# Kernel optimization log

Hardware: AMD Instinct MI355X
Metric: run time of the kernel (lower is better)

Reference implementation:

```python
import jax, jax.numpy as jnp
import numpy as np

N_NODES = 100000
N_EDGES = 1600000
IN_C, HID_C, OUT_C = 128, 128, 64


def setup_inputs() -> dict:
    key = jax.random.key(0)
    ks = jax.random.split(key, 8)
    x = jax.random.normal(ks[0], (N_NODES, IN_C), dtype=jnp.float32)
    edge_index = jax.random.randint(ks[1], (2, N_EDGES), 0, N_NODES, dtype=jnp.int32)
    # Glorot-ish init for GCNConv linear weights, zero bias (PyG default)
    def glorot(k, fan_in, fan_out):
        s = jnp.sqrt(6.0 / (fan_in + fan_out))
        return jax.random.uniform(k, (fan_in, fan_out), dtype=jnp.float32, minval=-s, maxval=s)
    return {
        "x": x,
        "edge_index": edge_index,
        "W1": glorot(ks[2], IN_C, HID_C), "b1": jnp.zeros((HID_C,), jnp.float32),
        "W2": glorot(ks[3], HID_C, HID_C), "b2": jnp.zeros((HID_C,), jnp.float32),
        "W3": glorot(ks[4], HID_C, OUT_C), "b3": jnp.zeros((OUT_C,), jnp.float32),
    }


def _gcn_norm(edge_index, num_nodes):
    # Add self-loops (PyG GCNConv default) and compute symmetric normalization
    loops = jnp.arange(num_nodes, dtype=edge_index.dtype)
    src = jnp.concatenate([edge_index[0], loops])  # [E+N]
    dst = jnp.concatenate([edge_index[1], loops])
    deg = jax.ops.segment_sum(jnp.ones_like(dst, dtype=jnp.float32), dst,
                              num_segments=num_nodes)
    deg_inv_sqrt = jnp.where(deg > 0, jax.lax.rsqrt(jnp.maximum(deg, 1.0)), 0.0)
    norm = deg_inv_sqrt[src] * deg_inv_sqrt[dst]  # [E+N]
    return src, dst, norm


def _gcn_layer(x, src, dst, norm, W, b, num_nodes):
    h = x @ W                                # [N, out] dense transform first
    msg = h[src] * norm[:, None]             # gather + scale  [E+N, out]
    out = jax.ops.segment_sum(msg, dst, num_segments=num_nodes)  # scatter-add
    return out + b


def reference(x, edge_index, W1, b1, W2, b2, W3, b3):
    n = x.shape[0]
    src, dst, norm = _gcn_norm(edge_index, n)
    h = jax.nn.relu(_gcn_layer(x, src, dst, norm, W1, b1, n))
    h = jax.nn.relu(_gcn_layer(h, src, dst, norm, W2, b2, n))
    return _gcn_layer(h, src, dst, norm, W3, b3, n)
```

## Files before the change

### kernel.cpp

```cpp
#include <hip/hip_runtime.h>

#define NN 100000
#define NE 1600000
#define NBK 98
#define BSH 10
#define MPAD 100096
#define SCB 391
#define CAP 20480

typedef unsigned short ushortT;
typedef unsigned long long ull;
using sh8 = __attribute__((ext_vector_type(8))) short;
using f4  = __attribute__((ext_vector_type(4))) float;


__device__ __forceinline__ unsigned short bfr(float f) {
  unsigned u = __float_as_uint(f);
  u += 0x7FFF + ((u >> 16) & 1);
  return (unsigned short)(u >> 16);
}
__device__ __forceinline__ float bf2f(unsigned short h) {
  return __uint_as_float(((unsigned)h) << 16);
}
__device__ __forceinline__ void acc8(const uint4 v, float* a) {
  a[0] += __uint_as_float(v.x << 16);
  a[1] += __uint_as_float(v.x & 0xFFFF0000u);
  a[2] += __uint_as_float(v.y << 16);
  a[3] += __uint_as_float(v.y & 0xFFFF0000u);
  a[4] += __uint_as_float(v.z << 16);
  a[5] += __uint_as_float(v.z & 0xFFFF0000u);
  a[6] += __uint_as_float(v.w << 16);
  a[7] += __uint_as_float(v.w & 0xFFFF0000u);
}
__device__ __forceinline__ sh8 hi8(const float4 a, const float4 b) {
  sh8 r;
  r[0] = (short)bfr(a.x); r[1] = (short)bfr(a.y);
  r[2] = (short)bfr(a.z); r[3] = (short)bfr(a.w);
  r[4] = (short)bfr(b.x); r[5] = (short)bfr(b.y);
  r[6] = (short)bfr(b.z); r[7] = (short)bfr(b.w);
  return r;
}


template <int COUT>
__device__ __forceinline__ void packone(const float* __restrict__ W,
                                        ushortT* __restrict__ Bp, int i) {
  const int j = i & 7;
  const int l = (i >> 3) & 63;
  const int rest = i >> 9;
  const int g = rest % (COUT / 16);
  const int ks = rest / (COUT / 16);
  const int k = (ks & 3) * 32 + (l >> 4) * 8 + j;
  const int n = g * 16 + (l & 15);
  const float v = W[k * COUT + n];
  const unsigned short h = bfr(v);
  Bp[i] = (ks < 4) ? h : bfr(v - bf2f(h));
}


__global__ __launch_bounds__(256) void k_scatterpack(
    const int* __restrict__ src, const int* __restrict__ dst,
    int* __restrict__ cursor, ull* __restrict__ pairArr,
    const float* __restrict__ W1, const float* __restrict__ W2,
    const float* __restrict__ W3, ushortT* __restrict__ Bp1,
    ushortT* __restrict__ Bp2, ushortT* __restrict__ Bp3) {
  if (blockIdx.x >= SCB) {
    const int i = (blockIdx.x - SCB) * 256 + threadIdx.x;
    if (i < 32768) packone<128>(W1, Bp1, i);
    else if (i < 65536) packone<128>(W2, Bp2, i - 32768);
    else packone<64>(W3, Bp3, i - 65536);
    return;
  }
  __shared__ int lcnt[NBK];
  __shared__ int lbase[NBK];
  __shared__ int lrank[NBK];
  __shared__ int bbase[NBK];
  __shared__ ull sorted[4096];
  __shared__ int target[4096];
  const int t = threadIdx.x;
  for (int i = t; i < NBK; i += 256) { lcnt[i] = 0; lrank[i] = 0; }
  __syncthreads();
  const int base = blockIdx.x * 4096;
  int rs[16], rd[16];
#pragma unroll
  for (int q = 0; q < 16; q++) {
    int e = base + t + 256 * q;
    rs[q] = (e < NE) ? src[e] : -1;
    rd[q] = (e < NE) ? dst[e] : -1;
    if (rd[q] >= 0) atomicAdd(&lcnt[rd[q] >> BSH], 1);
  }
  __syncthreads();
  if (t == 0) {
    int run = 0;
    for (int i = 0; i < NBK; i++) { lbase[i] = run; run += lcnt[i]; }
  }
  __syncthreads();
  if (t < NBK && lcnt[t] > 0) bbase[t] = atomicAdd(&cursor[t], lcnt[t]);
  __syncthreads();
#pragma unroll
  for (int q = 0; q < 16; q++) {
    if (rd[q] >= 0) {
      int b = rd[q] >> BSH;
      int r = atomicAdd(&lrank[b], 1);
      int slot = lbase[b] + r;
      sorted[slot] = ((ull)(unsigned)rs[q] << 32) | (unsigned)rd[q];
      target[slot] = b * CAP + bbase[b] + r;
    }
  }
  __syncthreads();
  const int n = min(4096, NE - base);
  for (int s = t; s < n; s += 256) pairArr[target[s]] = sorted[s];
}


__global__ __launch_bounds__(1024) void k_buildcsr(const ull* __restrict__ pairArr,
                                                   const int* __restrict__ cnt,
                                                   float* __restrict__ dinv,
                                                   int* __restrict__ rowptr,
                                                   int* __restrict__ col) {
  __shared__ int lc[1024];
  __shared__ int sd[1024];
  __shared__ int bc[NBK];
  __shared__ int ebegS;
  const int t = threadIdx.x;
  const int b = blockIdx.x;
  const int n0 = b << BSH;
  if (t < NBK) bc[t] = cnt[t];
  lc[t] = 0;
  __syncthreads();
  if (t == 0) {
    int run = 0;
    for (int i = 0; i < b; i++) run += bc[i];
    ebegS = run;
  }
  __syncthreads();
  const int ebeg = ebegS;
  const int myCnt = bc[b];
  const ull* pb = pairArr + (size_t)b * CAP;
  for (int i = t; i < myCnt; i += 1024)
    atomicAdd(&lc[(int)(unsigned)(pb[i] & 0xffffffffULL) - n0], 1);
  __syncthreads();
  const int v = lc[t];
  sd[t] = v;
  __syncthreads();
  for (int off = 1; off < 1024; off <<= 1) {
    int x = (t >= off) ? sd[t - off] : 0;
    __syncthreads();
    sd[t] += x;
    __syncthreads();
  }
  const int excl = sd[t] - v;
  lc[t] = excl;
  const int node = n0 + t;
  if (node < NN) {
    rowptr[node] = ebeg + excl;
    dinv[node] = rsqrtf(1.0f + (float)v);
  }
  if (b == 0 && t == 0) rowptr[NN] = NE;
  __syncthreads();
  for (int i = t; i < myCnt; i += 1024) {
    ull p = pb[i];
    int d = (int)(unsigned)(p & 0xffffffffULL);
    int srcv = (int)(unsigned)(p >> 32);
    int pos = atomicAdd(&lc[d - n0], 1);
    col[ebeg + pos] = srcv;
  }
}


template <int COUT, bool FUSED>
__global__ __launch_bounds__(256) void k_gemmM(const ushortT* __restrict__ A,
                                               const float* __restrict__ X,
                                               const ushortT* __restrict__ Bp,
                                               const float* __restrict__ dinv,
                                               ushortT* __restrict__ hs) {
  constexpr int CGALL = COUT / 16;
  constexpr int RG = 2;
  constexpr int CG = 4;
  const int w = threadIdx.x >> 6;
  const int lane = threadIdx.x & 63;
  const int q = lane >> 4;
  const int c = lane & 15;
  int row0, cg0;
  if (COUT == 128) {
    row0 = blockIdx.x * 64 + (w & 1) * 32;
    cg0 = (w >> 1) * 4;
  } else {
    row0 = blockIdx.x * 128 + w * 32;
    cg0 = 0;
  }

  const ushortT* ap[RG];
  const float* xp[RG];
#pragma unroll
  for (int rg = 0; rg < RG; rg++) {
    const int row = row0 + rg * 16 + c;
    if (FUSED) xp[rg] = X + (size_t)min(row, NN - 1) * 128 + q * 8;
    else ap[rg] = A + (size_t)row * 128 + q * 8;
  }
  const ushortT* bp0 = Bp + (size_t)lane * 8;

  f4 acc[RG][CG];
#pragma unroll
  for (int i = 0; i < RG; i++)
#pragma unroll
    for (int j = 0; j < CG; j++) acc[i][j] = (f4){0.f, 0.f, 0.f, 0.f};

  sh8 ah[RG], bh[CG], bl[CG];
  sh8 nah[RG], nbh[CG], nbl[CG];

  auto loadA = [&](int kr, sh8 (&h)[RG]) {
#pragma unroll
    for (int rg = 0; rg < RG; rg++) {
      if (FUSED) {
        const float4 x0 = *reinterpret_cast<const float4*>(xp[rg] + kr * 32);
        const float4 x1 = *reinterpret_cast<const float4*>(xp[rg] + kr * 32 + 4);
        h[rg] = hi8(x0, x1);
      } else {
        h[rg] = *reinterpret_cast<const sh8*>(ap[rg] + kr * 32);
      }
    }
  };
  auto loadB = [&](int kr, sh8 (&h)[CG], sh8 (&l)[CG]) {
#pragma unroll
    for (int cg = 0; cg < CG; cg++) {
      h[cg] = *reinterpret_cast<const sh8*>(bp0 + (size_t)(kr * CGALL + cg0 + cg) * 512);
      l[cg] = *reinterpret_cast<const sh8*>(bp0 + (size_t)((4 + kr) * CGALL + cg0 + cg) * 512);
    }
  };

  loadA(0, ah);
  loadB(0, bh, bl);
#pragma unroll
  for (int kr = 0; kr < 4; kr++) {
    if (kr < 3) {
      loadA(kr + 1, nah);
      loadB(kr + 1, nbh, nbl);
    }
#pragma unroll
    for (int rg = 0; rg < RG; rg++)
#pragma unroll
      for (int cg = 0; cg < CG; cg++)
        acc[rg][cg] = __builtin_amdgcn_mfma_f32_16x16x32_bf16(ah[rg], bh[cg],
                                                              acc[rg][cg], 0, 0, 0);
#pragma unroll
    for (int rg = 0; rg < RG; rg++)
#pragma unroll
      for (int cg = 0; cg < CG; cg++)
        acc[rg][cg] = __builtin_amdgcn_mfma_f32_16x16x32_bf16(ah[rg], bl[cg],
                                                              acc[rg][cg], 0, 0, 0);
    if (kr < 3) {
#pragma unroll
      for (int rg = 0; rg < RG; rg++) ah[rg] = nah[rg];
#pragma unroll
      for (int cg = 0; cg < CG; cg++) { bh[cg] = nbh[cg]; bl[cg] = nbl[cg]; }
    }
  }

#pragma unroll
  for (int rg = 0; rg < RG; rg++) {
#pragma unroll
    for (int reg = 0; reg < 4; reg++) {
      const int row = row0 + rg * 16 + q * 4 + reg;
      if (row < NN) {
        const float dv = dinv[row];
#pragma unroll
        for (int cg = 0; cg < CG; cg++) {
          hs[(size_t)row * COUT + (cg0 + cg) * 16 + c] = bfr(acc[rg][cg][reg] * dv);
        }
      }
    }
  }
}


template <bool RELU>
__global__ __launch_bounds__(256) void k_agg128(const ushortT* __restrict__ hs,
                                                const int* __restrict__ rowptr,
                                                const int* __restrict__ col,
                                                const float* __restrict__ dinv,
                                                const float* __restrict__ bias,
                                                ushortT* __restrict__ A) {
  const int gid = blockIdx.x * 256 + threadIdx.x;
  const int node = gid >> 6;
  if (node >= NN) return;
  const int lane = threadIdx.x & 63;
  const int q = lane >> 4;
  const int chb = (lane & 15) * 8;
  const int beg = rowptr[node];
  const int end = rowptr[node + 1];

  float a[8] = {};
  if (q == 0) {
    const uint4 v = *reinterpret_cast<const uint4*>(hs + (long)node * 128 + chb);
    acc8(v, a);
  }

  int j = beg;
  if (j + 8 <= end) {
    int c0 = col[j + q];
    int c1 = col[j + 4 + q];
    while (true) {
      const uint4 v0 = *reinterpret_cast<const uint4*>(hs + (long)c0 * 128 + chb);
      const uint4 v1 = *reinterpret_cast<const uint4*>(hs + (long)c1 * 128 + chb);
      j += 8;
      const bool more = (j + 8 <= end);
      int n0, n1;
      if (more) { n0 = col[j + q]; n1 = col[j + 4 + q]; }
      acc8(v0, a);
      acc8(v1, a);
      if (!more) break;
      c0 = n0; c1 = n1;
    }
  }
  for (; j + 4 <= end; j += 4) {
    int c = col[j + q];
    const uint4 v = *reinterpret_cast<const uint4*>(hs + (long)c * 128 + chb);
    acc8(v, a);
  }
  {
    const int r = end - j;
    if (q < r) {
      int c = col[j + q];
      const uint4 v = *reinterpret_cast<const uint4*>(hs + (long)c * 128 + chb);
      acc8(v, a);
    }
  }

#pragma unroll
  for (int i = 0; i < 8; i++) a[i] += __shfl(a[i], lane ^ 32);
#pragma unroll
  for (int i = 0; i < 8; i++) a[i] += __shfl(a[i], lane ^ 16);

  if (q == 0) {
    const float di = dinv[node];
    const float4 b0 = *reinterpret_cast<const float4*>(bias + chb);
    const float4 b1 = *reinterpret_cast<const float4*>(bias + chb + 4);
    float o[8];
    o[0] = fmaf(a[0], di, b0.x); o[1] = fmaf(a[1], di, b0.y);
    o[2] = fmaf(a[2], di, b0.z); o[3] = fmaf(a[3], di, b0.w);
    o[4] = fmaf(a[4], di, b1.x); o[5] = fmaf(a[5], di, b1.y);
    o[6] = fmaf(a[6], di, b1.z); o[7] = fmaf(a[7], di, b1.w);
    if (RELU) {
#pragma unroll
      for (int i = 0; i < 8; i++) o[i] = fmaxf(o[i], 0.f);
    }
    uint4 H;
    H.x = (unsigned)bfr(o[0]) | ((unsigned)bfr(o[1]) << 16);
    H.y = (unsigned)bfr(o[2]) | ((unsigned)bfr(o[3]) << 16);
    H.z = (unsigned)bfr(o[4]) | ((unsigned)bfr(o[5]) << 16);
    H.w = (unsigned)bfr(o[6]) | ((unsigned)bfr(o[7]) << 16);
    *reinterpret_cast<uint4*>(A + (long)node * 128 + chb) = H;
  }
}

__global__ __launch_bounds__(256) void k_agg64(const ushortT* __restrict__ hs,
                                               const int* __restrict__ rowptr,
                                               const int* __restrict__ col,
                                               const float* __restrict__ dinv,
                                               const float* __restrict__ bias,
                                               float* __restrict__ out) {
  const int gid = blockIdx.x * 256 + threadIdx.x;
  const int node = gid >> 6;
  if (node >= NN) return;
  const int lane = threadIdx.x & 63;
  const int o8 = lane >> 3;
  const int chb = (lane & 7) * 8;
  const int beg = rowptr[node];
  const int end = rowptr[node + 1];

  float a[8] = {};
  if (o8 == 0) {
    const uint4 v = *reinterpret_cast<const uint4*>(hs + (long)node * 64 + chb);
    acc8(v, a);
  }

  int j = beg;
  if (j + 16 <= end) {
    int c0 = col[j + o8];
    int c1 = col[j + 8 + o8];
    while (true) {
      const uint4 v0 = *reinterpret_cast<const uint4*>(hs + (long)c0 * 64 + chb);
      const uint4 v1 = *reinterpret_cast<const uint4*>(hs + (long)c1 * 64 + chb);
      j += 16;
      const bool more = (j + 16 <= end);
      int n0, n1;
      if (more) { n0 = col[j + o8]; n1 = col[j + 8 + o8]; }
      acc8(v0, a);
      acc8(v1, a);
      if (!more) break;
      c0 = n0; c1 = n1;
    }
  }
  for (; j + 8 <= end; j += 8) {
    int c = col[j + o8];
    const uint4 v = *reinterpret_cast<const uint4*>(hs + (long)c * 64 + chb);
    acc8(v, a);
  }
  {
    const int r = end - j;
    if (o8 < r) {
      int c = col[j + o8];
      const uint4 v = *reinterpret_cast<const uint4*>(hs + (long)c * 64 + chb);
      acc8(v, a);
    }
  }

#pragma unroll
  for (int i = 0; i < 8; i++) a[i] += __shfl(a[i], lane ^ 32);
#pragma unroll
  for (int i = 0; i < 8; i++) a[i] += __shfl(a[i], lane ^ 16);
#pragma unroll
  for (int i = 0; i < 8; i++) a[i] += __shfl(a[i], lane ^ 8);

  if (o8 == 0) {
    const float di = dinv[node];
    const float4 b0 = *reinterpret_cast<const float4*>(bias + chb);
    const float4 b1 = *reinterpret_cast<const float4*>(bias + chb + 4);
    float4 r0, r1;
    r0.x = fmaf(a[0], di, b0.x); r0.y = fmaf(a[1], di, b0.y);
    r0.z = fmaf(a[2], di, b0.z); r0.w = fmaf(a[3], di, b0.w);
    r1.x = fmaf(a[4], di, b1.x); r1.y = fmaf(a[5], di, b1.y);
    r1.z = fmaf(a[6], di, b1.z); r1.w = fmaf(a[7], di, b1.w);
    *reinterpret_cast<float4*>(out + (long)node * 64 + chb) = r0;
    *reinterpret_cast<float4*>(out + (long)node * 64 + chb + 4) = r1;
  }
}


extern "C" void kernel_launch(void* const* d_in, const int* in_sizes, int n_in,
                              void* d_out, int out_size, void* d_ws, size_t ws_size,
                              hipStream_t stream) {
  const float* x  = (const float*)d_in[0];
  const int* ei   = (const int*)d_in[1];
  const float* W1 = (const float*)d_in[2];
  const float* b1 = (const float*)d_in[3];
  const float* W2 = (const float*)d_in[4];
  const float* b2 = (const float*)d_in[5];
  const float* W3 = (const float*)d_in[6];
  const float* b3 = (const float*)d_in[7];
  float* out = (float*)d_out;
  const int* srcp = ei;
  const int* dstp = ei + NE;

  char* wsb = (char*)d_ws;
  size_t off = 0;
  auto alloc = [&](size_t bytes) -> void* {
    void* p = wsb + off;
    off += (bytes + 255) & ~(size_t)255;
    return p;
  };
  ushortT* A   = (ushortT*)alloc((size_t)MPAD * 128 * 2);
  ushortT* hs  = (ushortT*)alloc((size_t)NN * 128 * 2);
  int*   col    = (int*)alloc((size_t)NE * 4);
  int*   rowptr = (int*)alloc((size_t)(NN + 1) * 4);
  float* dinv   = (float*)alloc((size_t)NN * 4);
  int*   cursor = (int*)alloc((size_t)NBK * 4);
  ushortT* Bp1 = (ushortT*)alloc((size_t)32768 * 2);
  ushortT* Bp2 = (ushortT*)alloc((size_t)32768 * 2);
  ushortT* Bp3 = (ushortT*)alloc((size_t)16384 * 2);
  ull* pairArr = (ull*)hs;
  (void)ws_size; (void)in_sizes; (void)n_in; (void)out_size;

  hipMemsetAsync(cursor, 0, (size_t)NBK * 4, stream);
  k_scatterpack<<<SCB + 320, 256, 0, stream>>>(srcp, dstp, cursor, pairArr,
                                               W1, W2, W3, Bp1, Bp2, Bp3);
  k_buildcsr<<<NBK, 1024, 0, stream>>>(pairArr, cursor, dinv, rowptr, col);

  const int aggGrid = (NN * 64) / 256;
  const int gemmGrid128 = MPAD / 64;
  const int gemmGrid64 = MPAD / 128;

  k_gemmM<128, true><<<gemmGrid128, 256, 0, stream>>>(nullptr, x, Bp1, dinv, hs);
  k_agg128<true><<<aggGrid, 256, 0, stream>>>(hs, rowptr, col, dinv, b1, A);
  k_gemmM<128, false><<<gemmGrid128, 256, 0, stream>>>(A, nullptr, Bp2, dinv, hs);
  k_agg128<true><<<aggGrid, 256, 0, stream>>>(hs, rowptr, col, dinv, b2, A);
  k_gemmM<64, false><<<gemmGrid64, 256, 0, stream>>>(A, nullptr, Bp3, dinv, hs);
  k_agg64<<<aggGrid, 256, 0, stream>>>(hs, rowptr, col, dinv, b3, out);
}
```

Baseline: 371.7 us.

## Use finer CSR buckets, pack pairs into 32-bit words, unroll aggregation gather by 16

The CSR build now uses 391 buckets of 256 nodes instead of 98 buckets of 1024. Source and local destination are packed into a single 32-bit word, which halves the intermediate pair traffic. The buildcsr kernel runs more, smaller blocks and uses parallel scans and reductions in place of serial single-thread loops. The 128-wide aggregation loop is unrolled to keep 16 neighbor rows in flight, which raises memory-level parallelism at the cost of more registers.

```diff
diff --git a/kernel.cpp b/kernel.cpp
--- a/kernel.cpp
+++ b/kernel.cpp
@@ -2,11 +2,11 @@
 
 #define NN 100000
 #define NE 1600000
-#define NBK 98
-#define BSH 10
+#define NBK 391
+#define BSH 8
 #define MPAD 100096
 #define SCB 391
-#define CAP 20480
+#define CAP 5120
 
 typedef unsigned short ushortT;
 typedef unsigned long long ull;
@@ -60,7 +60,7 @@
 
 __global__ __launch_bounds__(256) void k_scatterpack(
     const int* __restrict__ src, const int* __restrict__ dst,
-    int* __restrict__ cursor, ull* __restrict__ pairArr,
+    int* __restrict__ cursor, unsigned* __restrict__ pairArr,
     const float* __restrict__ W1, const float* __restrict__ W2,
     const float* __restrict__ W3, ushortT* __restrict__ Bp1,
     ushortT* __restrict__ Bp2, ushortT* __restrict__ Bp3) {
@@ -71,14 +71,16 @@
     else packone<64>(W3, Bp3, i - 65536);
     return;
   }
-  __shared__ int lcnt[NBK];
-  __shared__ int lbase[NBK];
+  __shared__ int lcnt[512];
+  __shared__ int lbase[512];
   __shared__ int lrank[NBK];
   __shared__ int bbase[NBK];
-  __shared__ ull sorted[4096];
+  __shared__ int sd2[256];
+  __shared__ unsigned sorted[4096];
   __shared__ int target[4096];
   const int t = threadIdx.x;
-  for (int i = t; i < NBK; i += 256) { lcnt[i] = 0; lrank[i] = 0; }
+  for (int i = t; i < 512; i += 256) lcnt[i] = 0;
+  for (int i = t; i < NBK; i += 256) lrank[i] = 0;
   __syncthreads();
   const int base = blockIdx.x * 4096;
   int rs[16], rd[16];
@@ -90,12 +92,22 @@
     if (rd[q] >= 0) atomicAdd(&lcnt[rd[q] >> BSH], 1);
   }
   __syncthreads();
-  if (t == 0) {
-    int run = 0;
-    for (int i = 0; i < NBK; i++) { lbase[i] = run; run += lcnt[i]; }
-  }
-  __syncthreads();
-  if (t < NBK && lcnt[t] > 0) bbase[t] = atomicAdd(&cursor[t], lcnt[t]);
+  const int s0 = lcnt[2 * t];
+  const int s1 = lcnt[2 * t + 1];
+  sd2[t] = s0 + s1;
+  __syncthreads();
+  for (int off = 1; off < 256; off <<= 1) {
+    int x = (t >= off) ? sd2[t - off] : 0;
+    __syncthreads();
+    sd2[t] += x;
+    __syncthreads();
+  }
+  const int epair = sd2[t] - (s0 + s1);
+  lbase[2 * t] = epair;
+  lbase[2 * t + 1] = epair + s0;
+  __syncthreads();
+  for (int i = t; i < NBK; i += 256)
+    if (lcnt[i] > 0) bbase[i] = atomicAdd(&cursor[i], lcnt[i]);
   __syncthreads();
 #pragma unroll
   for (int q = 0; q < 16; q++) {
@@ -103,7 +115,7 @@
       int b = rd[q] >> BSH;
       int r = atomicAdd(&lrank[b], 1);
       int slot = lbase[b] + r;
-      sorted[slot] = ((ull)(unsigned)rs[q] << 32) | (unsigned)rd[q];
+      sorted[slot] = ((unsigned)rs[q] << 8) | ((unsigned)rd[q] & 255u);
       target[slot] = b * CAP + bbase[b] + r;
     }
   }
@@ -113,37 +125,39 @@
 }
 
 
-__global__ __launch_bounds__(1024) void k_buildcsr(const ull* __restrict__ pairArr,
-                                                   const int* __restrict__ cnt,
-                                                   float* __restrict__ dinv,
-                                                   int* __restrict__ rowptr,
-                                                   int* __restrict__ col) {
-  __shared__ int lc[1024];
-  __shared__ int sd[1024];
+__global__ __launch_bounds__(256) void k_buildcsr(const unsigned* __restrict__ pairArr,
+                                                  const int* __restrict__ cnt,
+                                                  float* __restrict__ dinv,
+                                                  int* __restrict__ rowptr,
+                                                  int* __restrict__ col) {
+  __shared__ int lc[256];
+  __shared__ int sd[256];
   __shared__ int bc[NBK];
-  __shared__ int ebegS;
   const int t = threadIdx.x;
   const int b = blockIdx.x;
   const int n0 = b << BSH;
-  if (t < NBK) bc[t] = cnt[t];
+  for (int i = t; i < NBK; i += 256) bc[i] = cnt[i];
   lc[t] = 0;
   __syncthreads();
-  if (t == 0) {
-    int run = 0;
-    for (int i = 0; i < b; i++) run += bc[i];
-    ebegS = run;
-  }
-  __syncthreads();
-  const int ebeg = ebegS;
+  int partial = 0;
+  for (int i = t; i < b; i += 256) partial += bc[i];
+  sd[t] = partial;
+  __syncthreads();
+  for (int off = 128; off > 0; off >>= 1) {
+    if (t < off) sd[t] += sd[t + off];
+    __syncthreads();
+  }
+  const int ebeg = sd[0];
   const int myCnt = bc[b];
-  const ull* pb = pairArr + (size_t)b * CAP;
-  for (int i = t; i < myCnt; i += 1024)
-    atomicAdd(&lc[(int)(unsigned)(pb[i] & 0xffffffffULL) - n0], 1);
+  __syncthreads();
+  const unsigned* pb = pairArr + (size_t)b * CAP;
+  for (int i = t; i < myCnt; i += 256)
+    atomicAdd(&lc[pb[i] & 255u], 1);
   __syncthreads();
   const int v = lc[t];
   sd[t] = v;
   __syncthreads();
-  for (int off = 1; off < 1024; off <<= 1) {
+  for (int off = 1; off < 256; off <<= 1) {
     int x = (t >= off) ? sd[t - off] : 0;
     __syncthreads();
     sd[t] += x;
@@ -158,11 +172,11 @@
   }
   if (b == 0 && t == 0) rowptr[NN] = NE;
   __syncthreads();
-  for (int i = t; i < myCnt; i += 1024) {
-    ull p = pb[i];
-    int d = (int)(unsigned)(p & 0xffffffffULL);
-    int srcv = (int)(unsigned)(p >> 32);
-    int pos = atomicAdd(&lc[d - n0], 1);
+  for (int i = t; i < myCnt; i += 256) {
+    unsigned p = pb[i];
+    int d = (int)(p & 255u);
+    int srcv = (int)(p >> 8);
+    int pos = atomicAdd(&lc[d], 1);
     col[ebeg + pos] = srcv;
   }
 }
@@ -297,26 +311,45 @@
   }
 
   int j = beg;
+  if (j + 16 <= end) {
+    int c0 = col[j + q];
+    int c1 = col[j + 4 + q];
+    int c2 = col[j + 8 + q];
+    int c3 = col[j + 12 + q];
+    while (true) {
+      const uint4 v0 = *reinterpret_cast<const uint4*>(hs + (long)c0 * 128 + chb);
+      const uint4 v1 = *reinterpret_cast<const uint4*>(hs + (long)c1 * 128 + chb);
+      const uint4 v2 = *reinterpret_cast<const uint4*>(hs + (long)c2 * 128 + chb);
+      const uint4 v3 = *reinterpret_cast<const uint4*>(hs + (long)c3 * 128 + chb);
+      j += 16;
+      const bool more = (j + 16 <= end);
+      int n0, n1, n2, n3;
+      if (more) {
+        n0 = col[j + q]; n1 = col[j + 4 + q];
+        n2 = col[j + 8 + q]; n3 = col[j + 12 + q];
+      }
+      acc8(v0, a);
+      acc8(v1, a);
+      acc8(v2, a);
+      acc8(v3, a);
+      if (!more) break;
+      c0 = n0; c1 = n1; c2 = n2; c3 = n3;
+    }
+  }
   if (j + 8 <= end) {
     int c0 = col[j + q];
     int c1 = col[j + 4 + q];
-    while (true) {
-      const uint4 v0 = *reinterpret_cast<const uint4*>(hs + (long)c0 * 128 + chb);
-      const uint4 v1 = *reinterpret_cast<const uint4*>(hs + (long)c1 * 128 + chb);
-      j += 8;
-      const bool more = (j + 8 <= end);
-      int n0, n1;
-      if (more) { n0 = col[j + q]; n1 = col[j + 4 + q]; }
-      acc8(v0, a);
-      acc8(v1, a);
-      if (!more) break;
-      c0 = n0; c1 = n1;
-    }
-  }
-  for (; j + 4 <= end; j += 4) {
+    const uint4 v0 = *reinterpret_cast<const uint4*>(hs + (long)c0 * 128 + chb);
+    const uint4 v1 = *reinterpret_cast<const uint4*>(hs + (long)c1 * 128 + chb);
+    acc8(v0, a);
+    acc8(v1, a);
+    j += 8;
+  }
+  if (j + 4 <= end) {
     int c = col[j + q];
     const uint4 v = *reinterpret_cast<const uint4*>(hs + (long)c * 128 + chb);
     acc8(v, a);
+    j += 4;
   }
   {
     const int r = end - j;
@@ -459,13 +492,13 @@
   ushortT* Bp1 = (ushortT*)alloc((size_t)32768 * 2);
   ushortT* Bp2 = (ushortT*)alloc((size_t)32768 * 2);
   ushortT* Bp3 = (ushortT*)alloc((size_t)16384 * 2);
-  ull* pairArr = (ull*)hs;
+  unsigned* pairArr = (unsigned*)hs;
   (void)ws_size; (void)in_sizes; (void)n_in; (void)out_size;
 
   hipMemsetAsync(cursor, 0, (size_t)NBK * 4, stream);
   k_scatterpack<<<SCB + 320, 256, 0, stream>>>(srcp, dstp, cursor, pairArr,
                                                W1, W2, W3, Bp1, Bp2, Bp3);
-  k_buildcsr<<<NBK, 1024, 0, stream>>>(pairArr, cursor, dinv, rowptr, col);
+  k_buildcsr<<<NBK, 256, 0, stream>>>(pairArr, cursor, dinv, rowptr, col);
 
   const int aggGrid = (NN * 64) / 256;
   const int gemmGrid128 = MPAD / 64;
```

Result: no change. 366.9 us (-1.3%).
